# Kernel optimization log

Measured on AMD Instinct MI355X. Metric: run time of the kernel, lower is better.

Reference implementation:

```python
import jax, jax.numpy as jnp
import numpy as np
import math

B, T, S = 32, 512, 256          # batch, tgt_len (prediction_length), src_len (encoder tokens)
PD, ED = 1, 768                 # pred_dim, encoder_dim
D, H, L, FF = 256, 8, 4, 1024   # d_model, nhead, num_layers, dim_feedforward
HD = D // H
NEG = -1e9
EPS = 1e-5


def _pos_encoding(seq_len, d_model):
    pos = jnp.arange(seq_len, dtype=jnp.float32)[:, None]
    div = jnp.exp(jnp.arange(0, d_model, 2, dtype=jnp.float32) * (-math.log(10000.0) / d_model))
    pe = jnp.zeros((seq_len, d_model), jnp.float32)
    pe = pe.at[:, 0::2].set(jnp.sin(pos * div))
    pe = pe.at[:, 1::2].set(jnp.cos(pos * div))
    return pe


def _ln(x, g, b):
    m = jnp.mean(x, -1, keepdims=True)
    v = jnp.mean((x - m) ** 2, -1, keepdims=True)
    return (x - m) * jax.lax.rsqrt(v + EPS) * g + b


def _mha(xq, xkv, Wq, bq, Wk, bk, Wv, bv, Wo, bo, mask):
    b, t, d = xq.shape
    s = xkv.shape[1]
    Q = (xq @ Wq + bq).reshape(b, t, H, HD).transpose(0, 2, 1, 3)   # bhtd
    K = (xkv @ Wk + bk).reshape(b, s, H, HD).transpose(0, 2, 1, 3)  # bhsd
    V = (xkv @ Wv + bv).reshape(b, s, H, HD).transpose(0, 2, 1, 3)
    scores = jnp.einsum('bhtd,bhsd->bhts', Q, K) * (HD ** -0.5)
    if mask is not None:
        scores = scores + mask
    w = jax.nn.softmax(scores, axis=-1)
    o = jnp.einsum('bhts,bhsd->bhtd', w, V).transpose(0, 2, 1, 3).reshape(b, t, d)
    return o @ Wo + bo


def _forward(tgt, memory, W_emb, b_emb, W_enc, b_enc,
             Wq_s, bq_s, Wk_s, bk_s, Wv_s, bv_s, Wo_s, bo_s,
             Wq_c, bq_c, Wk_c, bk_c, Wv_c, bv_c, Wo_c, bo_c,
             g1, be1, g2, be2, g3, be3, Wf1, bf1, Wf2, bf2,
             Wp1, bp1, Wp2, bp2):
    t = tgt.shape[1]
    x = tgt @ W_emb + b_emb + _pos_encoding(t, D)          # (B,T,D)
    mem = memory @ W_enc + b_enc                           # (B,S,D)
    causal = jnp.triu(jnp.full((t, t), NEG, jnp.float32), k=1)
    for i in range(L):
        sa = _mha(x, x, Wq_s[i], bq_s[i], Wk_s[i], bk_s[i], Wv_s[i], bv_s[i], Wo_s[i], bo_s[i], causal)
        x = _ln(x + sa, g1[i], be1[i])
        ca = _mha(x, mem, Wq_c[i], bq_c[i], Wk_c[i], bk_c[i], Wv_c[i], bv_c[i], Wo_c[i], bo_c[i], None)
        x = _ln(x + ca, g2[i], be2[i])
        ff = jax.nn.gelu(x @ Wf1[i] + bf1[i], approximate=False) @ Wf2[i] + bf2[i]
        x = _ln(x + ff, g3[i], be3[i])
    h = jax.nn.gelu(x @ Wp1 + bp1, approximate=False)
    return h @ Wp2 + bp2                                   # (B,T,PD)


def setup_inputs() -> dict:
    key = jax.random.key(0)
    keys = iter(jax.random.split(key, 40))
    def rn(shape, scale=0.05):
        return jax.random.normal(next(keys), shape, jnp.float32) * scale
    z = jnp.zeros
    inp = {
        'tgt': jax.random.normal(next(keys), (B, T, PD), jnp.float32),
        'memory': jax.random.normal(next(keys), (B, S, ED), jnp.float32),
        'W_emb': rn((PD, D)), 'b_emb': z((D,)),
        'W_enc': rn((ED, D)), 'b_enc': z((D,)),
        'Wq_s': rn((L, D, D)), 'bq_s': z((L, D)),
        'Wk_s': rn((L, D, D)), 'bk_s': z((L, D)),
        'Wv_s': rn((L, D, D)), 'bv_s': z((L, D)),
        'Wo_s': rn((L, D, D)), 'bo_s': z((L, D)),
        'Wq_c': rn((L, D, D)), 'bq_c': z((L, D)),
        'Wk_c': rn((L, D, D)), 'bk_c': z((L, D)),
        'Wv_c': rn((L, D, D)), 'bv_c': z((L, D)),
        'Wo_c': rn((L, D, D)), 'bo_c': z((L, D)),
        'g1': jnp.ones((L, D)), 'be1': z((L, D)),
        'g2': jnp.ones((L, D)), 'be2': z((L, D)),
        'g3': jnp.ones((L, D)), 'be3': z((L, D)),
        'Wf1': rn((L, D, FF)), 'bf1': z((L, FF)),
        'Wf2': rn((L, FF, D)), 'bf2': z((L, D)),
        'Wp1': rn((D, D // 2)), 'bp1': z((D // 2,)),
        'Wp2': rn((D // 2, PD), 0.01), 'bp2': jnp.full((PD,), 0.1, jnp.float32),
    }
    return inp


def reference(tgt, memory, W_emb, b_emb, W_enc, b_enc,
              Wq_s, bq_s, Wk_s, bk_s, Wv_s, bv_s, Wo_s, bo_s,
              Wq_c, bq_c, Wk_c, bk_c, Wv_c, bv_c, Wo_c, bo_c,
              g1, be1, g2, be2, g3, be3, Wf1, bf1, Wf2, bf2,
              Wp1, bp1, Wp2, bp2):
    return _forward(tgt, memory, W_emb, b_emb, W_enc, b_enc,
                    Wq_s, bq_s, Wk_s, bk_s, Wv_s, bv_s, Wo_s, bo_s,
                    Wq_c, bq_c, Wk_c, bk_c, Wv_c, bv_c, Wo_c, bo_c,
                    g1, be1, g2, be2, g3, be3, Wf1, bf1, Wf2, bf2,
                    Wp1, bp1, Wp2, bp2)
```

## Files before the change

### kernel.cpp

```cpp
#include <hip/hip_runtime.h>
#include <math.h>

#define B_  32
#define T_  512
#define S_  256
#define D_  256
#define H_  8
#define HD_ 32
#define FF_ 1024
#define ED_ 768
#define L_  4
#define BT_ (B_*T_)
#define BS_ (B_*S_)

typedef __bf16 bf16x8_t __attribute__((ext_vector_type(8)));
typedef __bf16 bf16x4_t __attribute__((ext_vector_type(4)));
typedef float  f32x4_t  __attribute__((ext_vector_type(4)));

__device__ __forceinline__ float gelu_f(float v) {
  return 0.5f * v * (1.f + erff(v * 0.7071067811865476f));
}

__device__ __forceinline__ void gl16(const __bf16* gsrc, __bf16* ldst) {
  __builtin_amdgcn_global_load_lds(
      (const __attribute__((address_space(1))) unsigned int*)gsrc,
      (__attribute__((address_space(3))) unsigned int*)ldst, 16, 0, 0);
}

__global__ __launch_bounds__(256)
void embed_kernel(const float* __restrict__ tgt, const float* __restrict__ Wemb,
                  const float* __restrict__ bemb, float* __restrict__ x,
                  __bf16* __restrict__ xbf) {
  int i = blockIdx.x * 256 + threadIdx.x;
  int d  = i & (D_ - 1);
  int bt = i >> 8;
  int t  = bt & (T_ - 1);
  int p  = d >> 1;
  float div = expf((float)(2 * p) * (-9.210340371976184f / (float)D_));
  float arg = (float)t * div;
  float pe = (d & 1) ? cosf(arg) : sinf(arg);
  float v = tgt[bt] * Wemb[d] + bemb[d] + pe;
  x[i] = v;
  xbf[i] = (__bf16)v;
}

__global__ __launch_bounds__(256)
void cvt_bf16_kernel(const float* __restrict__ in, __bf16* __restrict__ out) {
  int i = (blockIdx.x * 256 + threadIdx.x) * 4;
  float4 v = *(const float4*)(in + i);
  bf16x4_t o;
  o[0] = (__bf16)v.x; o[1] = (__bf16)v.y; o[2] = (__bf16)v.z; o[3] = (__bf16)v.w;
  *(bf16x4_t*)(out + i) = o;
}

struct TD { const float* src; size_t dst; int K, N, nb; size_t lstride; };
struct TDs { TD d[12]; };

__global__ __launch_bounds__(256)
void transpose_cvt_kernel(TDs a, __bf16* __restrict__ wt) {
  __shared__ float tile[32][33];
  TD t = a.d[blockIdx.y];
  const int kt = t.K >> 5, nt = t.N >> 5;
  const int per = kt * nt, tot = per * t.nb;
  const int id = blockIdx.x;
  if (id >= tot) return;
  const int b = id / per;
  const int r2 = id - b * per;
  const int kti = r2 / nt;
  const int nti = r2 - kti * nt;
  const int c = threadIdx.x & 31, r0 = threadIdx.x >> 5;
  const float* src = t.src + (size_t)b * t.K * t.N;
  __bf16* dst = wt + t.dst + (size_t)b * t.lstride;
#pragma unroll
  for (int j = 0; j < 4; ++j) {
    int rr = r0 + j * 8;
    tile[rr][c] = src[(size_t)(kti * 32 + rr) * t.N + nti * 32 + c];
  }
  __syncthreads();
#pragma unroll
  for (int j = 0; j < 4; ++j) {
    int rr = r0 + j * 8;
    dst[(size_t)(nti * 32 + rr) * t.K + kti * 32 + c] = (__bf16)tile[c][rr];
  }
}

__global__ __launch_bounds__(256)
void bias_concat_kernel(const float* __restrict__ bq_s, const float* __restrict__ bk_s,
                        const float* __restrict__ bv_s, const float* __restrict__ bk_c,
                        const float* __restrict__ bv_c, float* __restrict__ dst) {
  int idx = blockIdx.x * 256 + threadIdx.x;
  if (idx >= 5120) return;
  if (idx < 3072) {
    int l = idx / 768, c = idx - l * 768;
    float v = (c < 256) ? bq_s[l * 256 + c]
            : (c < 512) ? bk_s[l * 256 + c - 256]
                        : bv_s[l * 256 + c - 512];
    dst[idx] = v;
  } else {
    int j = idx - 3072;
    int l = j / 512, c = j - l * 512;
    float v = (c < 256) ? bk_c[l * 256 + c] : bv_c[l * 256 + c - 256];
    dst[idx] = v;
  }
}

template<int ACT, int OBF>
__global__ __launch_bounds__(256, 3)
void gemm_bf(const __bf16* __restrict__ A, const __bf16* __restrict__ Bt,
             const float* __restrict__ bias, void* __restrict__ Cv,
             int N, int K, int nN, int ppx) {
  __shared__ __bf16 As[128 * 64];
  __shared__ __bf16 Bs[64 * 64];
  const int tid = threadIdx.x, lane = tid & 63, wv = tid >> 6;
  const int wm = (wv & 1) * 64, wn = (wv >> 1) * 32;
  const int ln15 = lane & 15, kgrp = lane >> 4;
  const int xcd = blockIdx.x & 7, j = blockIdx.x >> 3;
  const int bm = (xcd * ppx + j / nN) * 128;
  const int bn = (j % nN) * 64;

  const int r8 = lane >> 3;
  const int scol = (lane & 7) ^ r8;
  const __bf16* a_g = A  + (size_t)(bm + wv * 32 + r8) * K + scol * 8;
  const __bf16* b_g = Bt + (size_t)(bn + wv * 16 + r8) * K + scol * 8;
  __bf16* a_l = As + wv * 2048;
  __bf16* b_l = Bs + wv * 1024;

  const int xk0 = kgrp ^ (ln15 & 7);
  const int xk1 = (4 + kgrp) ^ (ln15 & 7);

  f32x4_t acc[4][2];
#pragma unroll
  for (int mi = 0; mi < 4; ++mi)
#pragma unroll
    for (int ni = 0; ni < 2; ++ni) acc[mi][ni] = (f32x4_t){0.f, 0.f, 0.f, 0.f};

  for (int k0 = 0; k0 < K; k0 += 64) {
    gl16(a_g + k0,                a_l);
    gl16(a_g + k0 + (size_t)8*K,  a_l + 512);
    gl16(a_g + k0 + (size_t)16*K, a_l + 1024);
    gl16(a_g + k0 + (size_t)24*K, a_l + 1536);
    gl16(b_g + k0,                b_l);
    gl16(b_g + k0 + (size_t)8*K,  b_l + 512);
    __syncthreads();

#pragma unroll
    for (int kk = 0; kk < 2; ++kk) {
      const int xk = kk ? xk1 : xk0;
      bf16x8_t b0 = *(const bf16x8_t*)(Bs + ((wn + ln15) * 8 + xk) * 8);
      bf16x8_t b1 = *(const bf16x8_t*)(Bs + ((wn + 16 + ln15) * 8 + xk) * 8);
#pragma unroll
      for (int mi = 0; mi < 4; ++mi) {
        bf16x8_t af = *(const bf16x8_t*)(As + ((wm + mi * 16 + ln15) * 8 + xk) * 8);
        acc[mi][0] = __builtin_amdgcn_mfma_f32_16x16x32_bf16(af, b0, acc[mi][0], 0, 0, 0);
        acc[mi][1] = __builtin_amdgcn_mfma_f32_16x16x32_bf16(af, b1, acc[mi][1], 0, 0, 0);
      }
    }
    __syncthreads();
  }

#pragma unroll
  for (int mi = 0; mi < 4; ++mi) {
#pragma unroll
    for (int ni = 0; ni < 2; ++ni) {
      const int ocol = bn + wn + ni * 16 + ln15;
      const float bv = bias[ocol];
      const int orow0 = bm + wm + mi * 16 + kgrp * 4;
#pragma unroll
      for (int r = 0; r < 4; ++r) {
        float o = acc[mi][ni][r] + bv;
        if (ACT == 1) o = gelu_f(o);
        if (OBF) ((__bf16*)Cv)[(size_t)(orow0 + r) * N + ocol] = (__bf16)o;
        else     ((float*)Cv)[(size_t)(orow0 + r) * N + ocol] = o;
      }
    }
  }
}

template<int ACT, int OBF>
__global__ __launch_bounds__(256, 3)
void gemm_bf2(const __bf16* __restrict__ A, const __bf16* __restrict__ Bt,
              const float* __restrict__ bias, void* __restrict__ Cv,
              int N, int K, int nN, int ppx) {
  __shared__ __bf16 As[128 * 64];
  __shared__ __bf16 Bs[128 * 64];
  const int tid = threadIdx.x, lane = tid & 63, wv = tid >> 6;
  const int wm = (wv & 1) * 64, wn = (wv >> 1) * 64;
  const int ln15 = lane & 15, kgrp = lane >> 4;
  const int xcd = blockIdx.x & 7, j = blockIdx.x >> 3;
  const int bm = (xcd * ppx + j / nN) * 128;
  const int bn = (j % nN) * 128;

  const int r8 = lane >> 3;
  const int scol = (lane & 7) ^ r8;
  const __bf16* a_g = A  + (size_t)(bm + wv * 32 + r8) * K + scol * 8;
  const __bf16* b_g = Bt + (size_t)(bn + wv * 32 + r8) * K + scol * 8;
  __bf16* a_l = As + wv * 2048;
  __bf16* b_l = Bs + wv * 2048;

  const int xk0 = kgrp ^ (ln15 & 7);
  const int xk1 = (4 + kgrp) ^ (ln15 & 7);

  f32x4_t acc[4][4];
#pragma unroll
  for (int mi = 0; mi < 4; ++mi)
#pragma unroll
    for (int ni = 0; ni < 4; ++ni) acc[mi][ni] = (f32x4_t){0.f, 0.f, 0.f, 0.f};

  for (int k0 = 0; k0 < K; k0 += 64) {
    gl16(a_g + k0,                a_l);
    gl16(a_g + k0 + (size_t)8*K,  a_l + 512);
    gl16(a_g + k0 + (size_t)16*K, a_l + 1024);
    gl16(a_g + k0 + (size_t)24*K, a_l + 1536);
    gl16(b_g + k0,                b_l);
    gl16(b_g + k0 + (size_t)8*K,  b_l + 512);
    gl16(b_g + k0 + (size_t)16*K, b_l + 1024);
    gl16(b_g + k0 + (size_t)24*K, b_l + 1536);
    __syncthreads();

#pragma unroll
    for (int kk = 0; kk < 2; ++kk) {
      const int xk = kk ? xk1 : xk0;
      bf16x8_t bfr[4];
#pragma unroll
      for (int ni = 0; ni < 4; ++ni)
        bfr[ni] = *(const bf16x8_t*)(Bs + ((wn + ni * 16 + ln15) * 8 + xk) * 8);
#pragma unroll
      for (int mi = 0; mi < 4; ++mi) {
        bf16x8_t af = *(const bf16x8_t*)(As + ((wm + mi * 16 + ln15) * 8 + xk) * 8);
#pragma unroll
        for (int ni = 0; ni < 4; ++ni)
          acc[mi][ni] = __builtin_amdgcn_mfma_f32_16x16x32_bf16(af, bfr[ni], acc[mi][ni], 0, 0, 0);
      }
    }
    __syncthreads();
  }

#pragma unroll
  for (int mi = 0; mi < 4; ++mi) {
#pragma unroll
    for (int ni = 0; ni < 4; ++ni) {
      const int ocol = bn + wn + ni * 16 + ln15;
      const float bv = bias[ocol];
      const int orow0 = bm + wm + mi * 16 + kgrp * 4;
#pragma unroll
      for (int r = 0; r < 4; ++r) {
        float o = acc[mi][ni][r] + bv;
        if (ACT == 1) o = gelu_f(o);
        if (OBF) ((__bf16*)Cv)[(size_t)(orow0 + r) * N + ocol] = (__bf16)o;
        else     ((float*)Cv)[(size_t)(orow0 + r) * N + ocol] = o;
      }
    }
  }
}

__global__ __launch_bounds__(512)
void gemm_ln(const __bf16* __restrict__ A, const __bf16* __restrict__ Bt,
             const float* __restrict__ bias, const float* __restrict__ g,
             const float* __restrict__ bta, float* __restrict__ x,
             __bf16* __restrict__ xbf, int K, int ppx) {
  __shared__ __bf16 As[64 * 64];
  __shared__ __bf16 Bs[256 * 64];
  __shared__ float red[64][8];
  const int tid = threadIdx.x, lane = tid & 63, wv = tid >> 6;
  const int wm = (wv >> 2) * 32, wn = (wv & 3) * 64;
  const int ln15 = lane & 15, kgrp = lane >> 4;
  const int xcd = blockIdx.x & 7, j = blockIdx.x >> 3;
  const int bm = (xcd * ppx + j) * 64;

  const int sr = tid >> 3;
  const int sch = (tid & 7) ^ (sr & 7);
  const __bf16* a_g = A  + (size_t)(bm + sr) * K + sch * 8;
  const __bf16* b_g = Bt + (size_t)sr * K + sch * 8;
  __bf16* a_l = As + wv * 512;
  __bf16* b_l = Bs + wv * 512;

  const int xk0 = kgrp ^ (ln15 & 7);
  const int xk1 = (4 + kgrp) ^ (ln15 & 7);

  f32x4_t acc[2][4];
#pragma unroll
  for (int mi = 0; mi < 2; ++mi)
#pragma unroll
    for (int ni = 0; ni < 4; ++ni) acc[mi][ni] = (f32x4_t){0.f, 0.f, 0.f, 0.f};

  for (int k0 = 0; k0 < K; k0 += 64) {
    gl16(a_g + k0,                 a_l);
    gl16(b_g + k0,                 b_l);
    gl16(b_g + k0 + (size_t)64*K,  b_l + 4096);
    gl16(b_g + k0 + (size_t)128*K, b_l + 8192);
    gl16(b_g + k0 + (size_t)192*K, b_l + 12288);
    __syncthreads();

#pragma unroll
    for (int kk = 0; kk < 2; ++kk) {
      const int xk = kk ? xk1 : xk0;
      bf16x8_t bfr[4];
#pragma unroll
      for (int ni = 0; ni < 4; ++ni)
        bfr[ni] = *(const bf16x8_t*)(Bs + ((wn + ni * 16 + ln15) * 8 + xk) * 8);
#pragma unroll
      for (int mi = 0; mi < 2; ++mi) {
        bf16x8_t af = *(const bf16x8_t*)(As + ((wm + mi * 16 + ln15) * 8 + xk) * 8);
#pragma unroll
        for (int ni = 0; ni < 4; ++ni)
          acc[mi][ni] = __builtin_amdgcn_mfma_f32_16x16x32_bf16(af, bfr[ni], acc[mi][ni], 0, 0, 0);
      }
    }
    __syncthreads();
  }

  const int c0 = wn + ln15;
  float bs[4], gg[4], bb[4];
#pragma unroll
  for (int ni = 0; ni < 4; ++ni) {
    bs[ni] = bias[c0 + ni * 16];
    gg[ni] = g[c0 + ni * 16];
    bb[ni] = bta[c0 + ni * 16];
  }
  float v[2][4][4];
#pragma unroll
  for (int mi = 0; mi < 2; ++mi) {
#pragma unroll
    for (int r = 0; r < 4; ++r) {
      const int row = bm + wm + mi * 16 + kgrp * 4 + r;
      float s = 0.f, q = 0.f;
#pragma unroll
      for (int ni = 0; ni < 4; ++ni) {
        float t = acc[mi][ni][r] + bs[ni] + x[(size_t)row * 256 + c0 + ni * 16];
        v[mi][ni][r] = t; s += t; q += t * t;
      }
      s += __shfl_xor(s, 1); s += __shfl_xor(s, 2);
      s += __shfl_xor(s, 4); s += __shfl_xor(s, 8);
      q += __shfl_xor(q, 1); q += __shfl_xor(q, 2);
      q += __shfl_xor(q, 4); q += __shfl_xor(q, 8);
      if (ln15 == 0) {
        red[wm + mi * 16 + kgrp * 4 + r][(wv & 3) * 2 + 0] = s;
        red[wm + mi * 16 + kgrp * 4 + r][(wv & 3) * 2 + 1] = q;
      }
    }
  }
  __syncthreads();
#pragma unroll
  for (int mi = 0; mi < 2; ++mi) {
#pragma unroll
    for (int r = 0; r < 4; ++r) {
      const int rl = wm + mi * 16 + kgrp * 4 + r;
      const int row = bm + rl;
      const float ms = red[rl][0] + red[rl][2] + red[rl][4] + red[rl][6];
      const float mq = red[rl][1] + red[rl][3] + red[rl][5] + red[rl][7];
      const float mean = ms * (1.f / 256.f);
      const float var  = mq * (1.f / 256.f) - mean * mean;
      const float rstd = rsqrtf(fmaxf(var, 0.f) + 1e-5f);
#pragma unroll
      for (int ni = 0; ni < 4; ++ni) {
        float o = (v[mi][ni][r] - mean) * rstd * gg[ni] + bb[ni];
        x[(size_t)row * 256 + c0 + ni * 16] = o;
        xbf[(size_t)row * 256 + c0 + ni * 16] = (__bf16)o;
      }
    }
  }
}

template<bool CAUSAL>
__global__ __launch_bounds__(256)
void attn_mfma(const __bf16* __restrict__ Q, const __bf16* __restrict__ K,
               const __bf16* __restrict__ V, __bf16* __restrict__ O,
               int KVROWS, int qs, int ks) {
  const int b = blockIdx.x >> 3, h = blockIdx.x & 7;
  const int qt = blockIdx.y;
  const int tid = threadIdx.x, lane = tid & 63, wv = tid >> 6;
  const int ln15 = lane & 15, kgrp = lane >> 4, kgrp8 = kgrp * 8;

  __shared__ __bf16 K_lds[64][36];
  __shared__ __bf16 Vt_lds[32][72];
  __shared__ __bf16 P_lds[4][16][72];

  const int q_glob = qt * 64 + wv * 16 + ln15;
  const bf16x8_t qfrag = *(const bf16x8_t*)(Q + (size_t)(b * T_ + q_glob) * qs + h * HD_ + kgrp8);

  const int s_r = tid >> 2, s_c8 = (tid & 3) * 8;
  const __bf16* Kb = K + (size_t)(b * KVROWS + s_r) * ks + h * HD_ + s_c8;
  const __bf16* Vb = V + (size_t)(b * KVROWS + s_r) * ks + h * HD_ + s_c8;

  f32x4_t o0 = (f32x4_t){0.f,0.f,0.f,0.f}, o1 = (f32x4_t){0.f,0.f,0.f,0.f};
  float m = -3.0e38f, l = 0.f;
  const float SCALE = 0.17677669529663689f;
  const int slim = CAUSAL ? (qt + 1) * 64 : KVROWS;

  for (int s0 = 0; s0 < slim; s0 += 64) {
    *(bf16x8_t*)&K_lds[s_r][s_c8] = *(const bf16x8_t*)(Kb + (size_t)s0 * ks);
    bf16x8_t vv = *(const bf16x8_t*)(Vb + (size_t)s0 * ks);
#pragma unroll
    for (int jj = 0; jj < 8; ++jj) Vt_lds[s_c8 + jj][s_r] = vv[jj];
    __syncthreads();

    f32x4_t sa[4];
#pragma unroll
    for (int c = 0; c < 4; ++c) {
      bf16x8_t kf = *(const bf16x8_t*)&K_lds[c * 16 + ln15][kgrp8];
      sa[c] = __builtin_amdgcn_mfma_f32_16x16x32_bf16(kf, qfrag, (f32x4_t){0.f,0.f,0.f,0.f}, 0, 0, 0);
    }
    float v[16];
#pragma unroll
    for (int c = 0; c < 4; ++c)
#pragma unroll
      for (int r = 0; r < 4; ++r) {
        float s = sa[c][r] * SCALE;
        if (CAUSAL && (s0 + c * 16 + kgrp * 4 + r) > q_glob) s += -1e9f;
        v[c * 4 + r] = s;
      }
    float tmax = v[0];
#pragma unroll
    for (int r = 1; r < 16; ++r) tmax = fmaxf(tmax, v[r]);
    tmax = fmaxf(tmax, __shfl_xor(tmax, 16));
    tmax = fmaxf(tmax, __shfl_xor(tmax, 32));
    float mnew = fmaxf(m, tmax);
    float corr = __expf(m - mnew);

    float lsum = 0.f;
#pragma unroll
    for (int c = 0; c < 4; ++c) {
      bf16x4_t pc;
#pragma unroll
      for (int r = 0; r < 4; ++r) {
        float e = __expf(v[c * 4 + r] - mnew);
        lsum += e;
        pc[r] = (__bf16)e;
      }
      *(bf16x4_t*)&P_lds[wv][ln15][c * 16 + kgrp * 4] = pc;
    }
    lsum += __shfl_xor(lsum, 16);
    lsum += __shfl_xor(lsum, 32);
    l = l * corr + lsum;
    m = mnew;

    const float c0 = __shfl(corr, kgrp * 4 + 0);
    const float c1 = __shfl(corr, kgrp * 4 + 1);
    const float c2 = __shfl(corr, kgrp * 4 + 2);
    const float c3 = __shfl(corr, kgrp * 4 + 3);
    o0[0] *= c0; o0[1] *= c1; o0[2] *= c2; o0[3] *= c3;
    o1[0] *= c0; o1[1] *= c1; o1[2] *= c2; o1[3] *= c3;

    bf16x8_t pLo = *(const bf16x8_t*)&P_lds[wv][ln15][kgrp8];
    bf16x8_t pHi = *(const bf16x8_t*)&P_lds[wv][ln15][32 + kgrp8];
    bf16x8_t v0l = *(const bf16x8_t*)&Vt_lds[ln15][kgrp8];
    bf16x8_t v0h = *(const bf16x8_t*)&Vt_lds[ln15][32 + kgrp8];
    bf16x8_t v1l = *(const bf16x8_t*)&Vt_lds[16 + ln15][kgrp8];
    bf16x8_t v1h = *(const bf16x8_t*)&Vt_lds[16 + ln15][32 + kgrp8];
    o0 = __builtin_amdgcn_mfma_f32_16x16x32_bf16(pLo, v0l, o0, 0, 0, 0);
    o0 = __builtin_amdgcn_mfma_f32_16x16x32_bf16(pHi, v0h, o0, 0, 0, 0);
    o1 = __builtin_amdgcn_mfma_f32_16x16x32_bf16(pLo, v1l, o1, 0, 0, 0);
    o1 = __builtin_amdgcn_mfma_f32_16x16x32_bf16(pHi, v1h, o1, 0, 0, 0);
    __syncthreads();
  }

  const float inv = 1.f / l;
  const float i0 = __shfl(inv, kgrp * 4 + 0);
  const float i1 = __shfl(inv, kgrp * 4 + 1);
  const float i2 = __shfl(inv, kgrp * 4 + 2);
  const float i3 = __shfl(inv, kgrp * 4 + 3);
  __bf16* Op = O + (size_t)(b * T_ + qt * 64 + wv * 16 + kgrp * 4) * D_ + h * HD_;
  Op[0 * D_ + ln15] = (__bf16)(o0[0] * i0);  Op[0 * D_ + 16 + ln15] = (__bf16)(o1[0] * i0);
  Op[1 * D_ + ln15] = (__bf16)(o0[1] * i1);  Op[1 * D_ + 16 + ln15] = (__bf16)(o1[1] * i1);
  Op[2 * D_ + ln15] = (__bf16)(o0[2] * i2);  Op[2 * D_ + 16 + ln15] = (__bf16)(o1[2] * i2);
  Op[3 * D_ + ln15] = (__bf16)(o0[3] * i3);  Op[3 * D_ + 16 + ln15] = (__bf16)(o1[3] * i3);
}

__global__ __launch_bounds__(256)
void head2_kernel(const float* __restrict__ hb, const float* __restrict__ w,
                  const float* __restrict__ bias, float* __restrict__ out) {
  const int row = blockIdx.x * 4 + (threadIdx.x >> 6);
  const int lane = threadIdx.x & 63;
  float a = hb[(size_t)row * 128 + lane] * w[lane]
          + hb[(size_t)row * 128 + 64 + lane] * w[64 + lane];
#pragma unroll
  for (int off = 32; off; off >>= 1) a += __shfl_xor(a, off);
  if (lane == 0) out[row] = a + bias[0];
}

extern "C" void kernel_launch(void* const* d_in, const int* in_sizes, int n_in,
                              void* d_out, int out_size, void* d_ws, size_t ws_size,
                              hipStream_t stream) {
  const float* tgt    = (const float*)d_in[0];
  const float* memory = (const float*)d_in[1];
  const float* W_emb  = (const float*)d_in[2];
  const float* b_emb  = (const float*)d_in[3];
  const float* W_enc  = (const float*)d_in[4];
  const float* b_enc  = (const float*)d_in[5];
  const float* Wq_s = (const float*)d_in[6];  const float* bq_s = (const float*)d_in[7];
  const float* Wk_s = (const float*)d_in[8];  const float* bk_s = (const float*)d_in[9];
  const float* Wv_s = (const float*)d_in[10]; const float* bv_s = (const float*)d_in[11];
  const float* Wo_s = (const float*)d_in[12]; const float* bo_s = (const float*)d_in[13];
  const float* Wq_c = (const float*)d_in[14]; const float* bq_c = (const float*)d_in[15];
  const float* Wk_c = (const float*)d_in[16]; const float* bk_c = (const float*)d_in[17];
  const float* Wv_c = (const float*)d_in[18]; const float* bv_c = (const float*)d_in[19];
  const float* Wo_c = (const float*)d_in[20]; const float* bo_c = (const float*)d_in[21];
  const float* g1  = (const float*)d_in[22]; const float* be1 = (const float*)d_in[23];
  const float* g2  = (const float*)d_in[24]; const float* be2 = (const float*)d_in[25];
  const float* g3  = (const float*)d_in[26]; const float* be3 = (const float*)d_in[27];
  const float* Wf1 = (const float*)d_in[28]; const float* bf1 = (const float*)d_in[29];
  const float* Wf2 = (const float*)d_in[30]; const float* bf2 = (const float*)d_in[31];
  const float* Wp1 = (const float*)d_in[32]; const float* bp1 = (const float*)d_in[33];
  const float* Wp2 = (const float*)d_in[34]; const float* bp2 = (const float*)d_in[35];

  float*  x     = (float*)d_ws;
  __bf16* xbf   = (__bf16*)(x + (size_t)4194304);
  __bf16* membf = xbf + (size_t)4194304;
  __bf16* wt    = (__bf16*)((float*)membf + 1048576);
  float*  bcat  = (float*)(wt + 4423680);
  __bf16* kvall = (__bf16*)(bcat + 8192);
  __bf16* scr   = kvall + (size_t)16777216;
  __bf16* ao    = scr + (size_t)16777216;
  __bf16* memb = scr;
  __bf16* qkv  = scr;
  __bf16* qc   = scr;
  __bf16* ff   = scr;
  float*  hbuf = (float*)ao;

  const size_t o_enc  = 0;
  const size_t o_qkv  = 196608;
  const size_t o_qcw  = 983040;
  const size_t o_kvw  = 1245184;
  const size_t o_os   = 1769472;
  const size_t o_oc   = 2031616;
  const size_t o_f1   = 2293760;
  const size_t o_f2   = 3342336;
  const size_t o_p1   = 4390912;

  TDs td;
  td.d[0]  = {W_enc, o_enc,           ED_, D_,  1, 0};
  td.d[1]  = {Wq_s,  o_qkv + 0,       D_,  D_,  L_, 196608};
  td.d[2]  = {Wk_s,  o_qkv + 65536,   D_,  D_,  L_, 196608};
  td.d[3]  = {Wv_s,  o_qkv + 131072,  D_,  D_,  L_, 196608};
  td.d[4]  = {Wq_c,  o_qcw,           D_,  D_,  L_, 65536};
  td.d[5]  = {Wk_c,  o_kvw + 0,       D_,  D_,  L_, 131072};
  td.d[6]  = {Wv_c,  o_kvw + 65536,   D_,  D_,  L_, 131072};
  td.d[7]  = {Wo_s,  o_os,            D_,  D_,  L_, 65536};
  td.d[8]  = {Wo_c,  o_oc,            D_,  D_,  L_, 65536};
  td.d[9]  = {Wf1,   o_f1,            D_,  FF_, L_, 262144};
  td.d[10] = {Wf2,   o_f2,            FF_, D_,  L_, 262144};
  td.d[11] = {Wp1,   o_p1,            D_,  128, 1, 0};

  dim3 blk(256);
  cvt_bf16_kernel<<<BS_ * ED_ / 1024, blk, 0, stream>>>(memory, memb);
  transpose_cvt_kernel<<<dim3(1024, 12), blk, 0, stream>>>(td, wt);
  bias_concat_kernel<<<20, blk, 0, stream>>>(bq_s, bk_s, bv_s, bk_c, bv_c, bcat);
  embed_kernel<<<BT_ * D_ / 256, blk, 0, stream>>>(tgt, W_emb, b_emb, x, xbf);

  const float* bqkv = bcat;
  const float* bkv  = bcat + 3072;
  const dim3 gA(B_ * H_, T_ / 64);

  gemm_bf<0,1><<<64 * 4, blk, 0, stream>>>(memb, wt + o_enc, b_enc, membf, D_, ED_, 4, 8);
  gemm_bf2<0,1><<<64 * 16, blk, 0, stream>>>(membf, wt + o_kvw, bkv, kvall, 2048, D_, 16, 8);

  for (int i = 0; i < L_; ++i) {
    gemm_bf2<0,1><<<128 * 6, blk, 0, stream>>>(xbf, wt + o_qkv + (size_t)i * 196608, bqkv + i * 768, qkv, 768, D_, 6, 16);
    attn_mfma<true><<<gA, blk, 0, stream>>>(qkv, qkv + 256, qkv + 512, ao, T_, 768, 768);
    gemm_ln<<<256, dim3(512), 0, stream>>>(ao, wt + o_os + (size_t)i * 65536, bo_s + i * D_,
                                           g1 + i * D_, be1 + i * D_, x, xbf, D_, 32);
    gemm_bf<0,1><<<128 * 4, blk, 0, stream>>>(xbf, wt + o_qcw + (size_t)i * 65536, bq_c + i * D_, qc, D_, D_, 4, 16);
    attn_mfma<false><<<gA, blk, 0, stream>>>(qc, kvall + i * 512, kvall + i * 512 + 256, ao, S_, 256, 2048);
    gemm_ln<<<256, dim3(512), 0, stream>>>(ao, wt + o_oc + (size_t)i * 65536, bo_c + i * D_,
                                           g2 + i * D_, be2 + i * D_, x, xbf, D_, 32);
    gemm_bf2<1,1><<<128 * 8, blk, 0, stream>>>(xbf, wt + o_f1 + (size_t)i * 262144, bf1 + i * FF_, ff, FF_, D_, 8, 16);
    gemm_ln<<<256, dim3(512), 0, stream>>>(ff, wt + o_f2 + (size_t)i * 262144, bf2 + i * D_,
                                           g3 + i * D_, be3 + i * D_, x, xbf, FF_, 32);
  }
  gemm_bf<1,0><<<128 * 2, blk, 0, stream>>>(xbf, wt + o_p1, bp1, hbuf, 128, D_, 2, 16);
  head2_kernel<<<BT_ / 4, blk, 0, stream>>>(hbuf, Wp2, bp2, (float*)d_out);
}
```

Measured before the change: 697.4 us.

## Fuse following projection GEMM into LayerNorm GEMM epilogue

The GEMM+LayerNorm kernel now keeps the normalized 64-row tile in shared memory and immediately multiplies it by the next layer's weight: the cross-attention Q projection, FF1 with GELU, or the next layer's QKV projection. This removes three separate GEMM launches per layer and avoids re-reading xbf from global memory. Scratch buffers are split so qkv, ff, qc and ao no longer alias. In exchange, the fused kernel uses more shared memory (an extra 32KB tile) and only 256 blocks do the wide N=1024 and N=768 projections serially, which may cost parallelism compared with the standalone GEMMs that used 768 to 1024 blocks.

```diff
diff --git a/kernel.cpp b/kernel.cpp
--- a/kernel.cpp
+++ b/kernel.cpp
@@ -253,13 +253,17 @@
   }
 }
 
+template<int NEXT_N, int NACT>
 __global__ __launch_bounds__(512)
-void gemm_ln(const __bf16* __restrict__ A, const __bf16* __restrict__ Bt,
-             const float* __restrict__ bias, const float* __restrict__ g,
-             const float* __restrict__ bta, float* __restrict__ x,
-             __bf16* __restrict__ xbf, int K, int ppx) {
-  __shared__ __bf16 As[64 * 64];
-  __shared__ __bf16 Bs[256 * 64];
+void gemm_ln_next(const __bf16* __restrict__ A, const __bf16* __restrict__ Bt,
+                  const float* __restrict__ bias, const float* __restrict__ g,
+                  const float* __restrict__ bta, float* __restrict__ x,
+                  __bf16* __restrict__ xbf, int K, int ppx,
+                  const __bf16* __restrict__ Wn, const float* __restrict__ bn,
+                  __bf16* __restrict__ outn) {
+  __shared__ __bf16 As1[64 * 64];
+  __shared__ __bf16 Bs1[256 * 64];
+  __shared__ __bf16 An[64 * 256];
   __shared__ float red[64][8];
   const int tid = threadIdx.x, lane = tid & 63, wv = tid >> 6;
   const int wm = (wv >> 2) * 32, wn = (wv & 3) * 64;
@@ -271,8 +275,8 @@
   const int sch = (tid & 7) ^ (sr & 7);
   const __bf16* a_g = A  + (size_t)(bm + sr) * K + sch * 8;
   const __bf16* b_g = Bt + (size_t)sr * K + sch * 8;
-  __bf16* a_l = As + wv * 512;
-  __bf16* b_l = Bs + wv * 512;
+  __bf16* a_l = As1 + wv * 512;
+  __bf16* b_l = Bs1 + wv * 512;
 
   const int xk0 = kgrp ^ (ln15 & 7);
   const int xk1 = (4 + kgrp) ^ (ln15 & 7);
@@ -297,10 +301,10 @@
       bf16x8_t bfr[4];
 #pragma unroll
       for (int ni = 0; ni < 4; ++ni)
-        bfr[ni] = *(const bf16x8_t*)(Bs + ((wn + ni * 16 + ln15) * 8 + xk) * 8);
+        bfr[ni] = *(const bf16x8_t*)(Bs1 + ((wn + ni * 16 + ln15) * 8 + xk) * 8);
 #pragma unroll
       for (int mi = 0; mi < 2; ++mi) {
-        bf16x8_t af = *(const bf16x8_t*)(As + ((wm + mi * 16 + ln15) * 8 + xk) * 8);
+        bf16x8_t af = *(const bf16x8_t*)(As1 + ((wm + mi * 16 + ln15) * 8 + xk) * 8);
 #pragma unroll
         for (int ni = 0; ni < 4; ++ni)
           acc[mi][ni] = __builtin_amdgcn_mfma_f32_16x16x32_bf16(af, bfr[ni], acc[mi][ni], 0, 0, 0);
@@ -353,9 +357,71 @@
       const float rstd = rsqrtf(fmaxf(var, 0.f) + 1e-5f);
 #pragma unroll
       for (int ni = 0; ni < 4; ++ni) {
+        const int c = c0 + ni * 16;
         float o = (v[mi][ni][r] - mean) * rstd * gg[ni] + bb[ni];
-        x[(size_t)row * 256 + c0 + ni * 16] = o;
-        xbf[(size_t)row * 256 + c0 + ni * 16] = (__bf16)o;
+        x[(size_t)row * 256 + c] = o;
+        __bf16 ob = (__bf16)o;
+        xbf[(size_t)row * 256 + c] = ob;
+        if (NEXT_N > 0)
+          An[rl * 256 + (((c >> 3) ^ (rl & 7)) << 3) + (c & 7)] = ob;
+      }
+    }
+  }
+
+  if (NEXT_N > 0) {
+    const int r8l = lane >> 3;
+    const int scol2 = (lane & 7) ^ r8l;
+    __syncthreads();
+    for (int pass = 0; pass < NEXT_N / 256; ++pass) {
+      const int n0 = pass * 256;
+      f32x4_t a2[2][4];
+#pragma unroll
+      for (int mi = 0; mi < 2; ++mi)
+#pragma unroll
+        for (int ni = 0; ni < 4; ++ni) a2[mi][ni] = (f32x4_t){0.f, 0.f, 0.f, 0.f};
+
+      for (int k0 = 0; k0 < 256; k0 += 64) {
+        const __bf16* wsrc = Wn + (size_t)(n0 + wv * 8 + r8l) * 256 + k0 + scol2 * 8;
+        gl16(wsrc,                     Bs1 + wv * 512);
+        gl16(wsrc + (size_t)64 * 256,  Bs1 + 4096 + wv * 512);
+        gl16(wsrc + (size_t)128 * 256, Bs1 + 8192 + wv * 512);
+        gl16(wsrc + (size_t)192 * 256, Bs1 + 12288 + wv * 512);
+        __syncthreads();
+#pragma unroll
+        for (int kk = 0; kk < 2; ++kk) {
+          const int xkk = kk * 4 + kgrp;
+          bf16x8_t bfr[4];
+#pragma unroll
+          for (int ni = 0; ni < 4; ++ni) {
+            const int nl = wn + ni * 16 + ln15;
+            bfr[ni] = *(const bf16x8_t*)(Bs1 + (nl * 8 + (xkk ^ (nl & 7))) * 8);
+          }
+#pragma unroll
+          for (int mi = 0; mi < 2; ++mi) {
+            const int row = wm + mi * 16 + ln15;
+            const int ck = (k0 >> 3) + xkk;
+            bf16x8_t af = *(const bf16x8_t*)(An + row * 256 + ((ck ^ (row & 7)) << 3));
+#pragma unroll
+            for (int ni = 0; ni < 4; ++ni)
+              a2[mi][ni] = __builtin_amdgcn_mfma_f32_16x16x32_bf16(af, bfr[ni], a2[mi][ni], 0, 0, 0);
+          }
+        }
+        __syncthreads();
+      }
+#pragma unroll
+      for (int mi = 0; mi < 2; ++mi) {
+#pragma unroll
+        for (int ni = 0; ni < 4; ++ni) {
+          const int ocol = n0 + wn + ni * 16 + ln15;
+          const float b2 = bn[ocol];
+          const int orow0 = bm + wm + mi * 16 + kgrp * 4;
+#pragma unroll
+          for (int r = 0; r < 4; ++r) {
+            float o = a2[mi][ni][r] + b2;
+            if (NACT == 1) o = gelu_f(o);
+            outn[(size_t)(orow0 + r) * NEXT_N + ocol] = (__bf16)o;
+          }
+        }
       }
     }
   }
@@ -509,13 +575,12 @@
   __bf16* wt    = (__bf16*)((float*)membf + 1048576);
   float*  bcat  = (float*)(wt + 4423680);
   __bf16* kvall = (__bf16*)(bcat + 8192);
-  __bf16* scr   = kvall + (size_t)16777216;
-  __bf16* ao    = scr + (size_t)16777216;
-  __bf16* memb = scr;
-  __bf16* qkv  = scr;
-  __bf16* qc   = scr;
-  __bf16* ff   = scr;
-  float*  hbuf = (float*)ao;
+  __bf16* qkv   = kvall + (size_t)16777216;
+  __bf16* ff    = qkv + (size_t)12582912;
+  __bf16* qc    = ff + (size_t)16777216;
+  __bf16* ao    = qc + (size_t)4194304;
+  __bf16* memb = ff;
+  float*  hbuf = (float*)qc;
 
   const size_t o_enc  = 0;
   const size_t o_qkv  = 196608;
@@ -553,19 +618,26 @@
 
   gemm_bf<0,1><<<64 * 4, blk, 0, stream>>>(memb, wt + o_enc, b_enc, membf, D_, ED_, 4, 8);
   gemm_bf2<0,1><<<64 * 16, blk, 0, stream>>>(membf, wt + o_kvw, bkv, kvall, 2048, D_, 16, 8);
+  gemm_bf2<0,1><<<128 * 6, blk, 0, stream>>>(xbf, wt + o_qkv, bqkv, qkv, 768, D_, 6, 16);
 
   for (int i = 0; i < L_; ++i) {
-    gemm_bf2<0,1><<<128 * 6, blk, 0, stream>>>(xbf, wt + o_qkv + (size_t)i * 196608, bqkv + i * 768, qkv, 768, D_, 6, 16);
     attn_mfma<true><<<gA, blk, 0, stream>>>(qkv, qkv + 256, qkv + 512, ao, T_, 768, 768);
-    gemm_ln<<<256, dim3(512), 0, stream>>>(ao, wt + o_os + (size_t)i * 65536, bo_s + i * D_,
-                                           g1 + i * D_, be1 + i * D_, x, xbf, D_, 32);
-    gemm_bf<0,1><<<128 * 4, blk, 0, stream>>>(xbf, wt + o_qcw + (size_t)i * 65536, bq_c + i * D_, qc, D_, D_, 4, 16);
+    gemm_ln_next<256,0><<<256, dim3(512), 0, stream>>>(
+        ao, wt + o_os + (size_t)i * 65536, bo_s + i * D_, g1 + i * D_, be1 + i * D_,
+        x, xbf, D_, 32, wt + o_qcw + (size_t)i * 65536, bq_c + i * D_, qc);
     attn_mfma<false><<<gA, blk, 0, stream>>>(qc, kvall + i * 512, kvall + i * 512 + 256, ao, S_, 256, 2048);
-    gemm_ln<<<256, dim3(512), 0, stream>>>(ao, wt + o_oc + (size_t)i * 65536, bo_c + i * D_,
-                                           g2 + i * D_, be2 + i * D_, x, xbf, D_, 32);
-    gemm_bf2<1,1><<<128 * 8, blk, 0, stream>>>(xbf, wt + o_f1 + (size_t)i * 262144, bf1 + i * FF_, ff, FF_, D_, 8, 16);
-    gemm_ln<<<256, dim3(512), 0, stream>>>(ff, wt + o_f2 + (size_t)i * 262144, bf2 + i * D_,
-                                           g3 + i * D_, be3 + i * D_, x, xbf, FF_, 32);
+    gemm_ln_next<1024,1><<<256, dim3(512), 0, stream>>>(
+        ao, wt + o_oc + (size_t)i * 65536, bo_c + i * D_, g2 + i * D_, be2 + i * D_,
+        x, xbf, D_, 32, wt + o_f1 + (size_t)i * 262144, bf1 + i * FF_, ff);
+    if (i < L_ - 1) {
+      gemm_ln_next<768,0><<<256, dim3(512), 0, stream>>>(
+          ff, wt + o_f2 + (size_t)i * 262144, bf2 + i * D_, g3 + i * D_, be3 + i * D_,
+          x, xbf, FF_, 32, wt + o_qkv + (size_t)(i + 1) * 196608, bqkv + (i + 1) * 768, qkv);
+    } else {
+      gemm_ln_next<0,0><<<256, dim3(512), 0, stream>>>(
+          ff, wt + o_f2 + (size_t)i * 262144, bf2 + i * D_, g3 + i * D_, be3 + i * D_,
+          x, xbf, FF_, 32, (const __bf16*)nullptr, (const float*)nullptr, (__bf16*)nullptr);
+    }
   }
   gemm_bf<1,0><<<128 * 2, blk, 0, stream>>>(xbf, wt + o_p1, bp1, hbuf, 128, D_, 2, 16);
   head2_kernel<<<BT_ / 4, blk, 0, stream>>>(hbuf, Wp2, bp2, (float*)d_out);
```

Result: no change. 704.4 us (+1.0%).
